# Kernel tuning notes

Hardware: AMD Instinct MI355X
Metric: run time of the kernel (lower is better)

## Reference

```python
import jax, jax.numpy as jnp
import numpy as np

N_USERS = 100000
N_MOVIES = 50000
N_EDGES = 1000000
IN_CH, HID, OUT = 64, 128, 64


def setup_inputs() -> dict:
    key = jax.random.key(0)
    ks = jax.random.split(key, 8)
    N = N_USERS + N_MOVIES
    return {
        "edge_index": jax.random.randint(ks[0], (2, N_EDGES), 0, N, dtype=jnp.int64)
        if jax.config.jax_enable_x64 else jax.random.randint(ks[0], (2, N_EDGES), 0, N, dtype=jnp.int32),
        "user_emb": jax.random.normal(ks[1], (N_USERS, IN_CH), jnp.float32) * 0.05,
        "movie_emb": jax.random.normal(ks[2], (N_MOVIES, IN_CH), jnp.float32) * 0.05,
        "W1l": jax.random.normal(ks[3], (HID, IN_CH), jnp.float32) * 0.05,
        "b1": jnp.zeros((HID,), jnp.float32),
        "W1r": jax.random.normal(ks[4], (HID, IN_CH), jnp.float32) * 0.05,
        "W2l": jax.random.normal(ks[5], (OUT, HID), jnp.float32) * 0.05,
        "b2": jnp.zeros((OUT,), jnp.float32),
        "W2r": jax.random.normal(ks[6], (OUT, HID), jnp.float32) * 0.05,
    }


def _sage_conv(x, src, dst, Wl, bl, Wr, num_nodes):
    # mean-aggregate neighbor (source) features at destination nodes
    msg_sum = jax.ops.segment_sum(x[src], dst, num_segments=num_nodes)  # [N, d_in]
    deg = jax.ops.segment_sum(jnp.ones(src.shape, x.dtype), dst, num_segments=num_nodes)
    agg = msg_sum / jnp.maximum(deg, 1.0)[:, None]
    # out = lin_l(agg) + lin_r(x); lin_l carries the bias (PyG SAGEConv default)
    return agg @ Wl.T + bl + x @ Wr.T


def reference(edge_index, user_emb, movie_emb, W1l, b1, W1r, W2l, b2, W2r):
    N = user_emb.shape[0] + movie_emb.shape[0]
    src, dst = edge_index[0], edge_index[1]
    x = jnp.concatenate([user_emb, movie_emb], axis=0)  # [N, in_ch]
    x = jax.nn.relu(_sage_conv(x, src, dst, W1l, b1, W1r, N))  # dropout = identity (eval)
    x = _sage_conv(x, src, dst, W2l, b2, W2r, N)
    return x[:N_USERS], x[N_USERS:]
```

## Files before the change

kernel.cpp:

```cpp
#include <hip/hip_runtime.h>

constexpr int N_USERS  = 100000;
constexpr int N_MOVIES = 50000;
constexpr int N_NODES  = N_USERS + N_MOVIES;
constexpr int N_EDGES  = 1000000;
constexpr int CAP      = 32;

typedef __attribute__((ext_vector_type(8))) short bf16x8;
typedef __attribute__((ext_vector_type(8))) unsigned short usx8;
typedef __attribute__((ext_vector_type(4))) float f32x4;

__device__ inline unsigned short bf16_rne(float x) {
    unsigned u = __float_as_uint(x);
    unsigned r = (u + 0x7FFF + ((u >> 16) & 1)) >> 16;
    return (unsigned short)r;
}
__device__ inline float bf16_to_f(short v) {
    return __uint_as_float(((unsigned)(unsigned short)v) << 16);
}

constexpr int BUILD_BLKS = (N_EDGES / 8 + 255) / 256;
constexpr int PW_BLKS    = (2 * 128 * 128) / 256;
constexpr int PX_BLKS    = (N_NODES * 8 + 255) / 256;

__global__ __launch_bounds__(256) void prep_fused(const int* __restrict__ ei,
                                                  int* __restrict__ cnt,
                                                  int* __restrict__ srclist,
                                                  const float* __restrict__ W1l,
                                                  const float* __restrict__ W1r,
                                                  const float* __restrict__ W2l,
                                                  const float* __restrict__ W2r,
                                                  unsigned short* __restrict__ wb,
                                                  const float* __restrict__ ue,
                                                  const float* __restrict__ me,
                                                  unsigned short* __restrict__ xb) {
    const int ob = blockIdx.x;
    if (ob < BUILD_BLKS) {
        int t  = ob * 256 + threadIdx.x;
        int e0 = t * 8;
        if (e0 + 7 < N_EDGES) {
            int4 s0 = *(const int4*)&ei[e0];
            int4 s1 = *(const int4*)&ei[e0 + 4];
            int4 d0 = *(const int4*)&ei[N_EDGES + e0];
            int4 d1 = *(const int4*)&ei[N_EDGES + e0 + 4];
            int o[8];
            o[0] = atomicAdd(&cnt[d0.x], 1);
            o[1] = atomicAdd(&cnt[d0.y], 1);
            o[2] = atomicAdd(&cnt[d0.z], 1);
            o[3] = atomicAdd(&cnt[d0.w], 1);
            o[4] = atomicAdd(&cnt[d1.x], 1);
            o[5] = atomicAdd(&cnt[d1.y], 1);
            o[6] = atomicAdd(&cnt[d1.z], 1);
            o[7] = atomicAdd(&cnt[d1.w], 1);
            if (o[0] < CAP) srclist[(d0.x << 5) + o[0]] = s0.x;
            if (o[1] < CAP) srclist[(d0.y << 5) + o[1]] = s0.y;
            if (o[2] < CAP) srclist[(d0.z << 5) + o[2]] = s0.z;
            if (o[3] < CAP) srclist[(d0.w << 5) + o[3]] = s0.w;
            if (o[4] < CAP) srclist[(d1.x << 5) + o[4]] = s1.x;
            if (o[5] < CAP) srclist[(d1.y << 5) + o[5]] = s1.y;
            if (o[6] < CAP) srclist[(d1.z << 5) + o[6]] = s1.z;
            if (o[7] < CAP) srclist[(d1.w << 5) + o[7]] = s1.w;
        } else {
            for (int e = e0; e < N_EDGES; ++e) {
                int d = ei[N_EDGES + e];
                int o = atomicAdd(&cnt[d], 1);
                if (o < CAP) srclist[(d << 5) + o] = ei[e];
            }
        }
        return;
    }
    if (ob < BUILD_BLKS + PW_BLKS) {
        int i = (ob - BUILD_BLKS) * 256 + threadIdx.x;
        int layer = i >> 14;
        int r     = i & 16383;
        int kc    = r >> 12;
        int oc    = (r >> 9) & 7;
        int lane  = (r >> 3) & 63;
        int j     = r & 7;
        int k = kc * 32 + (lane >> 4) * 8 + j;
        int o = oc * 16 + (lane & 15);
        float v;
        if (layer == 0) v = (k < 64) ? W1l[o * 64 + k] : W1r[o * 64 + (k - 64)];
        else            v = (o < 64) ? W2l[o * 128 + k] : W2r[(o - 64) * 128 + k];
        wb[i] = bf16_rne(v);
        return;
    }
    int i = (ob - BUILD_BLKS - PW_BLKS) * 256 + threadIdx.x;
    if (i >= N_NODES * 8) return;
    int n = i >> 3, c = (i & 7) * 8;
    const float* src = (n < N_USERS) ? &ue[(size_t)n * 64 + c]
                                     : &me[(size_t)(n - N_USERS) * 64 + c];
    float4 v0 = *(const float4*)src;
    float4 v1 = *(const float4*)(src + 4);
    usx8 r;
    r[0] = bf16_rne(v0.x); r[1] = bf16_rne(v0.y);
    r[2] = bf16_rne(v0.z); r[3] = bf16_rne(v0.w);
    r[4] = bf16_rne(v1.x); r[5] = bf16_rne(v1.y);
    r[6] = bf16_rne(v1.z); r[7] = bf16_rne(v1.w);
    *(usx8*)&xb[(size_t)n * 64 + c] = r;
}

__global__ __launch_bounds__(256) void gather1(const int* __restrict__ cnt,
                                               const int* __restrict__ srclist,
                                               const unsigned short* __restrict__ xb,
                                               unsigned short* __restrict__ aggb) {
    int gid = blockIdx.x * 256 + threadIdx.x;
    int n = gid >> 3, l = gid & 7;
    if (n >= N_NODES) return;
    int deg = cnt[n];
    float acc[8] = {};
    for (int i = 0; i < deg; ++i) {
        int a = srclist[(n << 5) + i];
        bf16x8 v = *(const bf16x8*)&xb[(size_t)a * 64 + l * 8];
#pragma unroll
        for (int j = 0; j < 8; ++j) acc[j] += bf16_to_f(v[j]);
    }
    float inv = 1.0f / fmaxf((float)deg, 1.0f);
    usx8 r;
#pragma unroll
    for (int j = 0; j < 8; ++j) r[j] = bf16_rne(acc[j] * inv);
    *(usx8*)&aggb[(size_t)n * 64 + l * 8] = r;
}

__global__ __launch_bounds__(256) void gather2_final(const int* __restrict__ cnt,
                                                     const int* __restrict__ srclist,
                                                     const unsigned short* __restrict__ zb,
                                                     const unsigned short* __restrict__ wfb,
                                                     float* __restrict__ out) {
    int gid = blockIdx.x * 256 + threadIdx.x;
    int n = gid >> 3, l = gid & 7;
    if (n >= N_NODES) return;
    int deg = cnt[n];
    float acc[8] = {};
    for (int i = 0; i < deg; ++i) {
        int a = srclist[(n << 5) + i];
        bf16x8 v = *(const bf16x8*)&zb[(size_t)a * 64 + l * 8];
#pragma unroll
        for (int j = 0; j < 8; ++j) acc[j] += bf16_to_f(v[j]);
    }
    float inv = 1.0f / fmaxf((float)deg, 1.0f);
    bf16x8 wv = *(const bf16x8*)&wfb[(size_t)n * 64 + l * 8];
    float4 r0, r1;
    r0.x = acc[0] * inv + bf16_to_f(wv[0]);
    r0.y = acc[1] * inv + bf16_to_f(wv[1]);
    r0.z = acc[2] * inv + bf16_to_f(wv[2]);
    r0.w = acc[3] * inv + bf16_to_f(wv[3]);
    r1.x = acc[4] * inv + bf16_to_f(wv[4]);
    r1.y = acc[5] * inv + bf16_to_f(wv[5]);
    r1.z = acc[6] * inv + bf16_to_f(wv[6]);
    r1.w = acc[7] * inv + bf16_to_f(wv[7]);
    *(float4*)&out[(size_t)n * 64 + l * 8]     = r0;
    *(float4*)&out[(size_t)n * 64 + l * 8 + 4] = r1;
}

__global__ __launch_bounds__(256) void gemm_fused(const unsigned short* __restrict__ aggb,
                                                  const unsigned short* __restrict__ xb,
                                                  const unsigned short* __restrict__ wb,
                                                  const float* __restrict__ b1,
                                                  const float* __restrict__ b2,
                                                  unsigned short* __restrict__ zb,
                                                  unsigned short* __restrict__ wfb) {
    __shared__ unsigned short hs[128][136];
    const int tid  = threadIdx.x;
    const int w    = tid >> 6;
    const int lane = tid & 63;
    const int n0   = blockIdx.x * 128;
    const int nw   = n0 + w * 32;
    const int lr   = lane & 15;
    const int lg   = lane >> 4;

    {
        f32x4 acc[2][8] = {};
        for (int kc = 0; kc < 4; ++kc) {
            const int k0 = kc * 32 + lg * 8;
            bf16x8 a[2];
#pragma unroll
            for (int f = 0; f < 2; ++f) {
                int node = nw + f * 16 + lr;
                bf16x8 z = {};
                a[f] = z;
                if (node < N_NODES) {
                    const unsigned short* ap = (k0 < 64)
                        ? &aggb[(size_t)node * 64 + k0]
                        : &xb[(size_t)node * 64 + (k0 - 64)];
                    a[f] = *(const bf16x8*)ap;
                }
            }
#pragma unroll
            for (int oc = 0; oc < 8; ++oc) {
                size_t widx = ((size_t)((kc * 8 + oc) * 64 + lane)) * 8;
                bf16x8 wfrag = *(const bf16x8*)&wb[widx];
#pragma unroll
                for (int f = 0; f < 2; ++f)
                    acc[f][oc] = __builtin_amdgcn_mfma_f32_16x16x32_bf16(a[f], wfrag, acc[f][oc], 0, 0, 0);
            }
        }
#pragma unroll
        for (int f = 0; f < 2; ++f) {
#pragma unroll
            for (int oc = 0; oc < 8; ++oc) {
                int col = oc * 16 + lr;
                float b = b1[col];
#pragma unroll
                for (int i = 0; i < 4; ++i) {
                    int rowl = w * 32 + f * 16 + lg * 4 + i;
                    hs[rowl][col] = bf16_rne(fmaxf(acc[f][oc][i] + b, 0.f));
                }
            }
        }
    }
    __syncthreads();

    {
        f32x4 acc[2][8] = {};
        for (int kc = 0; kc < 4; ++kc) {
            const int k0 = kc * 32 + lg * 8;
            bf16x8 a[2];
#pragma unroll
            for (int f = 0; f < 2; ++f) {
                int rowl = w * 32 + f * 16 + lr;
                a[f] = *(const bf16x8*)&hs[rowl][k0];
            }
#pragma unroll
            for (int oc = 0; oc < 8; ++oc) {
                size_t widx = ((size_t)(2048 + (kc * 8 + oc) * 64 + lane)) * 8;
                bf16x8 wfrag = *(const bf16x8*)&wb[widx];
#pragma unroll
                for (int f = 0; f < 2; ++f)
                    acc[f][oc] = __builtin_amdgcn_mfma_f32_16x16x32_bf16(a[f], wfrag, acc[f][oc], 0, 0, 0);
            }
        }
#pragma unroll
        for (int f = 0; f < 2; ++f) {
#pragma unroll
            for (int oc = 0; oc < 8; ++oc) {
                int col = oc * 16 + lr;
                float badd = (oc < 4) ? 0.f : b2[col - 64];
#pragma unroll
                for (int i = 0; i < 4; ++i) {
                    int row = nw + f * 16 + lg * 4 + i;
                    if (row < N_NODES) {
                        unsigned short v = bf16_rne(acc[f][oc][i] + badd);
                        if (oc < 4) zb[(size_t)row * 64 + col] = v;
                        else        wfb[(size_t)row * 64 + (col - 64)] = v;
                    }
                }
            }
        }
    }
}

extern "C" void kernel_launch(void* const* d_in, const int* in_sizes, int n_in,
                              void* d_out, int out_size, void* d_ws, size_t ws_size,
                              hipStream_t stream) {
    const int*   ei  = (const int*)d_in[0];
    const float* ue  = (const float*)d_in[1];
    const float* me  = (const float*)d_in[2];
    const float* W1l = (const float*)d_in[3];
    const float* b1  = (const float*)d_in[4];
    const float* W1r = (const float*)d_in[5];
    const float* W2l = (const float*)d_in[6];
    const float* b2  = (const float*)d_in[7];
    const float* W2r = (const float*)d_in[8];
    float* out = (float*)d_out;

    char* p = (char*)d_ws;
    int* srclist = (int*)p;                   p += (size_t)N_NODES * CAP * 4;
    int* cnt     = (int*)p;                   p += ((N_NODES * 4) + 255) / 256 * 256;
    unsigned short* wb  = (unsigned short*)p; p += 2 * 128 * 128 * 2;
    unsigned short* xb  = (unsigned short*)p; p += (size_t)N_NODES * 64 * 2;
    unsigned short* zb  = (unsigned short*)p; p += (size_t)N_NODES * 64 * 2;
    unsigned short* wfb = (unsigned short*)p; p += (size_t)N_NODES * 64 * 2;
    unsigned short* aggb = (unsigned short*)out;

    hipMemsetAsync(cnt, 0, N_NODES * sizeof(int), stream);
    prep_fused<<<BUILD_BLKS + PW_BLKS + PX_BLKS, 256, 0, stream>>>(
        ei, cnt, srclist, W1l, W1r, W2l, W2r, wb, ue, me, xb);

    int gblocks = (N_NODES * 8 + 255) / 256;
    int mblocks = (N_NODES + 127) / 128;

    gather1<<<gblocks, 256, 0, stream>>>(cnt, srclist, xb, aggb);
    gemm_fused<<<mblocks, 256, 0, stream>>>(aggb, xb, wb, b1, b2, zb, wfb);
    gather2_final<<<gblocks, 256, 0, stream>>>(cnt, srclist, zb, wfb, out);
}
```

Measured before the change: 188.9 us.

## Split CSR build into atomic slot-reservation pass and separate scatter kernel

The adjacency build no longer does its scattered srclist writes in the same threads that issue the atomics. The first pass now only reserves each edge's slot with an atomic and stores that offset coherently to an ord array. A new kernel then reads source, destination and offset and scatters into srclist. The gather loops now clamp degree to CAP, which also fixes reads past a node's slot list when its degree exceeds CAP. The split avoids stalling the scatter stores on atomic return latency, but adds an extra launch and a 4MB ord write and read.

Result: faster. 176.9 us (-6.4%).

```diff
diff --git a/kernel.cpp b/kernel.cpp
--- a/kernel.cpp
+++ b/kernel.cpp
@@ -19,13 +19,13 @@
     return __uint_as_float(((unsigned)(unsigned short)v) << 16);
 }
 
-constexpr int BUILD_BLKS = (N_EDGES / 8 + 255) / 256;
-constexpr int PW_BLKS    = (2 * 128 * 128) / 256;
-constexpr int PX_BLKS    = (N_NODES * 8 + 255) / 256;
+constexpr int ORD_BLKS = (N_EDGES / 8 + 255) / 256;
+constexpr int PW_BLKS  = (2 * 128 * 128) / 256;
+constexpr int PX_BLKS  = (N_NODES * 8 + 255) / 256;
 
 __global__ __launch_bounds__(256) void prep_fused(const int* __restrict__ ei,
                                                   int* __restrict__ cnt,
-                                                  int* __restrict__ srclist,
+                                                  int* __restrict__ ord,
                                                   const float* __restrict__ W1l,
                                                   const float* __restrict__ W1r,
                                                   const float* __restrict__ W2l,
@@ -35,42 +35,31 @@
                                                   const float* __restrict__ me,
                                                   unsigned short* __restrict__ xb) {
     const int ob = blockIdx.x;
-    if (ob < BUILD_BLKS) {
+    if (ob < ORD_BLKS) {
         int t  = ob * 256 + threadIdx.x;
         int e0 = t * 8;
         if (e0 + 7 < N_EDGES) {
-            int4 s0 = *(const int4*)&ei[e0];
-            int4 s1 = *(const int4*)&ei[e0 + 4];
             int4 d0 = *(const int4*)&ei[N_EDGES + e0];
             int4 d1 = *(const int4*)&ei[N_EDGES + e0 + 4];
-            int o[8];
-            o[0] = atomicAdd(&cnt[d0.x], 1);
-            o[1] = atomicAdd(&cnt[d0.y], 1);
-            o[2] = atomicAdd(&cnt[d0.z], 1);
-            o[3] = atomicAdd(&cnt[d0.w], 1);
-            o[4] = atomicAdd(&cnt[d1.x], 1);
-            o[5] = atomicAdd(&cnt[d1.y], 1);
-            o[6] = atomicAdd(&cnt[d1.z], 1);
-            o[7] = atomicAdd(&cnt[d1.w], 1);
-            if (o[0] < CAP) srclist[(d0.x << 5) + o[0]] = s0.x;
-            if (o[1] < CAP) srclist[(d0.y << 5) + o[1]] = s0.y;
-            if (o[2] < CAP) srclist[(d0.z << 5) + o[2]] = s0.z;
-            if (o[3] < CAP) srclist[(d0.w << 5) + o[3]] = s0.w;
-            if (o[4] < CAP) srclist[(d1.x << 5) + o[4]] = s1.x;
-            if (o[5] < CAP) srclist[(d1.y << 5) + o[5]] = s1.y;
-            if (o[6] < CAP) srclist[(d1.z << 5) + o[6]] = s1.z;
-            if (o[7] < CAP) srclist[(d1.w << 5) + o[7]] = s1.w;
+            int4 o0, o1;
+            o0.x = atomicAdd(&cnt[d0.x], 1);
+            o0.y = atomicAdd(&cnt[d0.y], 1);
+            o0.z = atomicAdd(&cnt[d0.z], 1);
+            o0.w = atomicAdd(&cnt[d0.w], 1);
+            o1.x = atomicAdd(&cnt[d1.x], 1);
+            o1.y = atomicAdd(&cnt[d1.y], 1);
+            o1.z = atomicAdd(&cnt[d1.z], 1);
+            o1.w = atomicAdd(&cnt[d1.w], 1);
+            *(int4*)&ord[e0]     = o0;
+            *(int4*)&ord[e0 + 4] = o1;
         } else {
-            for (int e = e0; e < N_EDGES; ++e) {
-                int d = ei[N_EDGES + e];
-                int o = atomicAdd(&cnt[d], 1);
-                if (o < CAP) srclist[(d << 5) + o] = ei[e];
-            }
+            for (int e = e0; e < N_EDGES; ++e)
+                ord[e] = atomicAdd(&cnt[ei[N_EDGES + e]], 1);
         }
         return;
     }
-    if (ob < BUILD_BLKS + PW_BLKS) {
-        int i = (ob - BUILD_BLKS) * 256 + threadIdx.x;
+    if (ob < ORD_BLKS + PW_BLKS) {
+        int i = (ob - ORD_BLKS) * 256 + threadIdx.x;
         int layer = i >> 14;
         int r     = i & 16383;
         int kc    = r >> 12;
@@ -85,7 +74,7 @@
         wb[i] = bf16_rne(v);
         return;
     }
-    int i = (ob - BUILD_BLKS - PW_BLKS) * 256 + threadIdx.x;
+    int i = (ob - ORD_BLKS - PW_BLKS) * 256 + threadIdx.x;
     if (i >= N_NODES * 8) return;
     int n = i >> 3, c = (i & 7) * 8;
     const float* src = (n < N_USERS) ? &ue[(size_t)n * 64 + c]
@@ -100,6 +89,27 @@
     *(usx8*)&xb[(size_t)n * 64 + c] = r;
 }
 
+__global__ __launch_bounds__(256) void csr_scatter(const int* __restrict__ ei,
+                                                   const int* __restrict__ ord,
+                                                   int* __restrict__ srclist) {
+    int t  = blockIdx.x * 256 + threadIdx.x;
+    int e0 = t * 4;
+    if (e0 + 3 < N_EDGES) {
+        int4 s = *(const int4*)&ei[e0];
+        int4 d = *(const int4*)&ei[N_EDGES + e0];
+        int4 o = *(const int4*)&ord[e0];
+        if (o.x < CAP) srclist[(d.x << 5) + o.x] = s.x;
+        if (o.y < CAP) srclist[(d.y << 5) + o.y] = s.y;
+        if (o.z < CAP) srclist[(d.z << 5) + o.z] = s.z;
+        if (o.w < CAP) srclist[(d.w << 5) + o.w] = s.w;
+    } else {
+        for (int e = e0; e < N_EDGES; ++e) {
+            int o = ord[e];
+            if (o < CAP) srclist[(ei[N_EDGES + e] << 5) + o] = ei[e];
+        }
+    }
+}
+
 __global__ __launch_bounds__(256) void gather1(const int* __restrict__ cnt,
                                                const int* __restrict__ srclist,
                                                const unsigned short* __restrict__ xb,
@@ -108,8 +118,9 @@
     int n = gid >> 3, l = gid & 7;
     if (n >= N_NODES) return;
     int deg = cnt[n];
+    int m = min(deg, CAP);
     float acc[8] = {};
-    for (int i = 0; i < deg; ++i) {
+    for (int i = 0; i < m; ++i) {
         int a = srclist[(n << 5) + i];
         bf16x8 v = *(const bf16x8*)&xb[(size_t)a * 64 + l * 8];
 #pragma unroll
@@ -131,8 +142,9 @@
     int n = gid >> 3, l = gid & 7;
     if (n >= N_NODES) return;
     int deg = cnt[n];
+    int m = min(deg, CAP);
     float acc[8] = {};
-    for (int i = 0; i < deg; ++i) {
+    for (int i = 0; i < m; ++i) {
         int a = srclist[(n << 5) + i];
         bf16x8 v = *(const bf16x8*)&zb[(size_t)a * 64 + l * 8];
 #pragma unroll
@@ -267,6 +279,7 @@
     char* p = (char*)d_ws;
     int* srclist = (int*)p;                   p += (size_t)N_NODES * CAP * 4;
     int* cnt     = (int*)p;                   p += ((N_NODES * 4) + 255) / 256 * 256;
+    int* ord     = (int*)p;                   p += (size_t)N_EDGES * 4;
     unsigned short* wb  = (unsigned short*)p; p += 2 * 128 * 128 * 2;
     unsigned short* xb  = (unsigned short*)p; p += (size_t)N_NODES * 64 * 2;
     unsigned short* zb  = (unsigned short*)p; p += (size_t)N_NODES * 64 * 2;
@@ -274,8 +287,9 @@
     unsigned short* aggb = (unsigned short*)out;
 
     hipMemsetAsync(cnt, 0, N_NODES * sizeof(int), stream);
-    prep_fused<<<BUILD_BLKS + PW_BLKS + PX_BLKS, 256, 0, stream>>>(
-        ei, cnt, srclist, W1l, W1r, W2l, W2r, wb, ue, me, xb);
+    prep_fused<<<ORD_BLKS + PW_BLKS + PX_BLKS, 256, 0, stream>>>(
+        ei, cnt, ord, W1l, W1r, W2l, W2r, wb, ue, me, xb);
+    csr_scatter<<<(N_EDGES / 4 + 255) / 256, 256, 0, stream>>>(ei, ord, srclist);
 
     int gblocks = (N_NODES * 8 + 255) / 256;
     int mblocks = (N_NODES + 127) / 128;
```
